# Optimization experiments

Hardware: AMD Instinct MI355X
Metric: run time of the kernel (lower is better)

## Reference

```python
import jax, jax.numpy as jnp
import numpy as np

HID = 1024
NEG = -1e10


def setup_inputs() -> dict:
    key = jax.random.key(0)
    ks = jax.random.split(key, 8)
    batch, src_len = 64, 512
    hidden = jax.random.normal(ks[0], (batch, HID), dtype=jnp.float32)
    encoder_outputs = jax.random.normal(ks[1], (src_len, batch, 2 * HID), dtype=jnp.float32)
    mask = jax.random.randint(ks[2], (batch, src_len), 0, 2).astype(bool)
    # params (torch Linear: y = x @ W.T + b)
    sW = 1.0 / np.sqrt(HID)
    sU = 1.0 / np.sqrt(2 * HID)
    W_w = jax.random.uniform(ks[3], (HID, HID), jnp.float32, -sW, sW)
    W_b = jax.random.uniform(ks[4], (HID,), jnp.float32, -sW, sW)
    U_w = jax.random.uniform(ks[5], (HID, 2 * HID), jnp.float32, -sU, sU)
    U_b = jax.random.uniform(ks[6], (HID,), jnp.float32, -sU, sU)
    v_w = jax.random.uniform(ks[7], (1, HID), jnp.float32, -sW, sW)
    return {"hidden": hidden, "encoder_outputs": encoder_outputs, "mask": mask,
            "W_w": W_w, "W_b": W_b, "U_w": U_w, "U_b": U_b, "v_w": v_w}


def reference(hidden, encoder_outputs, mask, W_w, W_b, U_w, U_b, v_w):
    # hidden: [B, H]; encoder_outputs: [S, B, 2H]; mask: [B, S]
    Wh = hidden @ W_w.T + W_b                       # [B, H], broadcast over S
    enc = jnp.transpose(encoder_outputs, (1, 0, 2))  # [B, S, 2H]
    Ue = jnp.einsum('bse,he->bsh', enc, U_w) + U_b   # [B, S, H]
    energy = jnp.tanh(Wh[:, None, :] + Ue) @ v_w[0]  # [B, S]
    energy = jnp.where(mask, NEG, energy)
    return jax.nn.softmax(energy, axis=1)
```

## Files before the change

### kernel.cpp

```cpp
#include <hip/hip_runtime.h>
#include <math.h>

#define HID   1024
#define HID2  2048
#define BATCH 64
#define SRC   512
#define MROWS (SRC * BATCH)
#define NEGV  (-1e10f)

typedef int  i4v __attribute__((ext_vector_type(4)));
typedef float f4v __attribute__((ext_vector_type(4)));

__global__ void zero_energy(float* __restrict__ e) {
    int i = blockIdx.x * 256 + threadIdx.x;
    if (i < MROWS) e[i] = 0.f;
}

__global__ void split_i8(const float* __restrict__ src,
                         signed char* __restrict__ q1b,
                         signed char* __restrict__ q2b,
                         int n16, float s1, float inv_s1, float s2) {
    int i = blockIdx.x * 256 + threadIdx.x;
    if (i >= n16) return;
    const float4* s = (const float4*)src + (size_t)i * 4;
    float v[16];
    *(float4*)&v[0]  = s[0];
    *(float4*)&v[4]  = s[1];
    *(float4*)&v[8]  = s[2];
    *(float4*)&v[12] = s[3];
    unsigned w1[4], w2[4];
#pragma unroll
    for (int p = 0; p < 4; ++p) {
        unsigned a1 = 0, a2 = 0;
#pragma unroll
        for (int j = 0; j < 4; ++j) {
            float a  = v[p * 4 + j];
            float q1 = rintf(a * s1);
            q1 = fminf(fmaxf(q1, -127.f), 127.f);
            float r  = fmaf(q1, -inv_s1, a);
            float q2 = rintf(r * s2);
            q2 = fminf(fmaxf(q2, -127.f), 127.f);
            a1 |= ((unsigned)((int)q1 & 0xff)) << (8 * j);
            a2 |= ((unsigned)((int)q2 & 0xff)) << (8 * j);
        }
        w1[p] = a1; w2[p] = a2;
    }
    ((uint4*)q1b)[i] = make_uint4(w1[0], w1[1], w1[2], w1[3]);
    ((uint4*)q2b)[i] = make_uint4(w2[0], w2[1], w2[2], w2[3]);
}

__global__ void quant_i8(const float* __restrict__ src,
                         signed char* __restrict__ qb,
                         int n16, float s) {
    int i = blockIdx.x * 256 + threadIdx.x;
    if (i >= n16) return;
    const float4* sp = (const float4*)src + (size_t)i * 4;
    float v[16];
    *(float4*)&v[0]  = sp[0];
    *(float4*)&v[4]  = sp[1];
    *(float4*)&v[8]  = sp[2];
    *(float4*)&v[12] = sp[3];
    unsigned w[4];
#pragma unroll
    for (int p = 0; p < 4; ++p) {
        unsigned a = 0;
#pragma unroll
        for (int j = 0; j < 4; ++j) {
            float q = rintf(v[p * 4 + j] * s);
            q = fminf(fmaxf(q, -127.f), 127.f);
            a |= ((unsigned)((int)q & 0xff)) << (8 * j);
        }
        w[p] = a;
    }
    ((uint4*)qb)[i] = make_uint4(w[0], w[1], w[2], w[3]);
}

__global__ void wh_kernel(const float* __restrict__ hidden,
                          const float* __restrict__ W_w,
                          const float* __restrict__ W_b,
                          float* __restrict__ Wh) {
    __shared__ float sh[HID];
    const int b = blockIdx.y;
    const int t = threadIdx.x;
    for (int k = t; k < HID; k += 256) sh[k] = hidden[b * HID + k];
    __syncthreads();
    const int h = blockIdx.x * 256 + t;
    const float* wr = W_w + (size_t)h * HID;
    float acc = 0.f;
    for (int k = 0; k < HID; k += 4) {
        float4 w = *(const float4*)(wr + k);
        acc += sh[k] * w.x + sh[k+1] * w.y + sh[k+2] * w.z + sh[k+3] * w.w;
    }
    Wh[b * HID + h] = acc + W_b[h];
}

static __device__ __forceinline__ float tanh_fast(float x) {
    float ax = fabsf(x);
    float t  = __expf(-2.f * ax);
    float r  = __fdividef(1.f - t, 1.f + t);
    return copysignf(r, x);
}

__global__ __launch_bounds__(256, 2)
void gemm_energy(const signed char* __restrict__ A1,
                 const signed char* __restrict__ A2,
                 const signed char* __restrict__ B1,
                 const float* __restrict__ Ub,
                 const float* __restrict__ vw,
                 const float* __restrict__ Wh,
                 float* __restrict__ energy,
                 int m_base)
{
    __shared__ signed char sA1[128 * 64];
    __shared__ signed char sA2[128 * 64];
    __shared__ signed char sB1[128 * 64];

    const int tid  = threadIdx.x;
    const int wave = tid >> 6;
    const int lane = tid & 63;

    const int nwg = (int)(gridDim.x * gridDim.y);
    const int bid = (int)(blockIdx.y * gridDim.x + blockIdx.x);
    const int cpx = nwg >> 3;
    const int swz = (bid & 7) * cpx + (bid >> 3);
    const int h0 = (swz & 7) * 128;
    const int m0 = (swz >> 3) * 128;

    const int wm = wave & 1;
    const int wn = wave >> 1;

    i4v c1[4][4], c2[4][4];
#pragma unroll
    for (int i = 0; i < 4; i++)
#pragma unroll
        for (int j = 0; j < 4; j++) {
            c1[i][j] = (i4v){0, 0, 0, 0};
            c2[i][j] = (i4v){0, 0, 0, 0};
        }

    const int ar   = lane & 15;
    const int koff = (lane >> 4) * 16;

    for (int k0 = 0; k0 < HID2; k0 += 64) {
#pragma unroll
        for (int it = 0; it < 2; ++it) {
            const int f    = it * 256 + tid;
            const int row  = f >> 2;
            const int inn  = (f & 3) * 16;
            const int loff = (it * 256 + wave * 64) * 16;

            const signed char* ga = A1 + (size_t)(m0 + row) * HID2 + k0 + inn;
            __builtin_amdgcn_global_load_lds(
                (const __attribute__((address_space(1))) unsigned int*)ga,
                (__attribute__((address_space(3))) unsigned int*)(sA1 + loff),
                16, 0, 0);
            const signed char* gb = A2 + (size_t)(m0 + row) * HID2 + k0 + inn;
            __builtin_amdgcn_global_load_lds(
                (const __attribute__((address_space(1))) unsigned int*)gb,
                (__attribute__((address_space(3))) unsigned int*)(sA2 + loff),
                16, 0, 0);
            const signed char* gc = B1 + (size_t)(h0 + row) * HID2 + k0 + inn;
            __builtin_amdgcn_global_load_lds(
                (const __attribute__((address_space(1))) unsigned int*)gc,
                (__attribute__((address_space(3))) unsigned int*)(sB1 + loff),
                16, 0, 0);
        }
        __syncthreads();

        i4v a1[4], a2[4], b1[4];
#pragma unroll
        for (int i = 0; i < 4; ++i) {
            a1[i] = *(const i4v*)&sA1[(wm * 64 + i * 16 + ar) * 64 + koff];
            a2[i] = *(const i4v*)&sA2[(wm * 64 + i * 16 + ar) * 64 + koff];
            b1[i] = *(const i4v*)&sB1[(wn * 64 + i * 16 + ar) * 64 + koff];
        }
#pragma unroll
        for (int i = 0; i < 4; ++i)
#pragma unroll
            for (int j = 0; j < 4; ++j) {
                c1[i][j] = __builtin_amdgcn_mfma_i32_16x16x64_i8(a1[i], b1[j], c1[i][j], 0, 0, 0);
                c2[i][j] = __builtin_amdgcn_mfma_i32_16x16x64_i8(a2[i], b1[j], c2[i][j], 0, 0, 0);
            }
        __syncthreads();
    }

    const int col = lane & 15;
    const int rg  = lane >> 4;
    const float invs = 1.f / (4096.f * 5746.f);
    float vj[4], ubj[4];
#pragma unroll
    for (int j = 0; j < 4; ++j) {
        const int hc = h0 + wn * 64 + j * 16 + col;
        vj[j]  = vw[hc];
        ubj[j] = Ub[hc];
    }
#pragma unroll
    for (int i = 0; i < 4; ++i) {
#pragma unroll
        for (int r = 0; r < 4; ++r) {
            const int mm = m0 + wm * 64 + i * 16 + rg * 4 + r;
            const int b  = (m_base + mm) & 63;
            const float* whr = Wh + b * HID + h0 + wn * 64 + col;
            float e = 0.f;
#pragma unroll
            for (int j = 0; j < 4; ++j) {
                float C = fmaf((float)c1[i][j][r], 256.f, (float)c2[i][j][r]) * invs;
                float x = C + ubj[j] + whr[j * 16];
                e += vj[j] * tanh_fast(x);
            }
            e += __shfl_xor(e, 1, 64);
            e += __shfl_xor(e, 2, 64);
            e += __shfl_xor(e, 4, 64);
            e += __shfl_xor(e, 8, 64);
            if (col == 0) atomicAdd(&energy[m_base + mm], e);
        }
    }
}

__global__ void softmax_kernel(const float* __restrict__ energy,
                               const int* __restrict__ mask,
                               float* __restrict__ out) {
    const int b = blockIdx.x;
    const int t = threadIdx.x;
    __shared__ float wmax[4], wsum[4];

    float x0 = energy[t * 64 + b];
    float x1 = energy[(t + 256) * 64 + b];
    float e0 = mask[b * SRC + t]       ? NEGV : x0;
    float e1 = mask[b * SRC + t + 256] ? NEGV : x1;

    float mx = fmaxf(e0, e1);
#pragma unroll
    for (int off = 1; off < 64; off <<= 1)
        mx = fmaxf(mx, __shfl_xor(mx, off, 64));
    const int wid = t >> 6, lane = t & 63;
    if (lane == 0) wmax[wid] = mx;
    __syncthreads();
    mx = fmaxf(fmaxf(wmax[0], wmax[1]), fmaxf(wmax[2], wmax[3]));

    float p0 = expf(e0 - mx), p1 = expf(e1 - mx);
    float sum = p0 + p1;
#pragma unroll
    for (int off = 1; off < 64; off <<= 1)
        sum += __shfl_xor(sum, off, 64);
    if (lane == 0) wsum[wid] = sum;
    __syncthreads();
    sum = wsum[0] + wsum[1] + wsum[2] + wsum[3];
    const float inv = 1.f / sum;
    out[b * SRC + t]       = p0 * inv;
    out[b * SRC + t + 256] = p1 * inv;
}

extern "C" void kernel_launch(void* const* d_in, const int* in_sizes, int n_in,
                              void* d_out, int out_size, void* d_ws, size_t ws_size,
                              hipStream_t stream) {
    const float* hidden = (const float*)d_in[0];
    const float* enc    = (const float*)d_in[1];
    const int*   mask   = (const int*)d_in[2];
    const float* W_w    = (const float*)d_in[3];
    const float* W_b    = (const float*)d_in[4];
    const float* U_w    = (const float*)d_in[5];
    const float* U_b    = (const float*)d_in[6];
    const float* v_w    = (const float*)d_in[7];
    float* out = (float*)d_out;

    char* p = (char*)d_ws;
    float* Wh     = (float*)p;             p += (size_t)BATCH * HID * 4;
    float* energy = (float*)p;             p += (size_t)MROWS * 4;
    signed char* B1 = (signed char*)p;     p += (size_t)HID * HID2;
    const size_t fixed = (size_t)(p - (char*)d_ws);

    int R = 1024;
    const int cand[6] = {32768, 16384, 8192, 4096, 2048, 1024};
    for (int c = 0; c < 6; ++c) {
        if (fixed + (size_t)cand[c] * HID2 * 2 <= ws_size) { R = cand[c]; break; }
    }
    signed char* A1 = (signed char*)p;
    signed char* A2 = A1 + (size_t)R * HID2;

    const float Sa1 = 16.f, iSa1 = 1.f / 16.f, Sa2 = 4096.f;
    const float Sb1 = 5746.f;

    hipLaunchKernelGGL(zero_energy, dim3(MROWS / 256), dim3(256), 0, stream, energy);
    hipLaunchKernelGGL(wh_kernel, dim3(4, BATCH), dim3(256), 0, stream,
                       hidden, W_w, W_b, Wh);
    {
        const int n16 = HID * HID2 / 16;
        hipLaunchKernelGGL(quant_i8, dim3((n16 + 255) / 256), dim3(256), 0, stream,
                           U_w, B1, n16, Sb1);
    }
    for (int c0 = 0; c0 < MROWS; c0 += R) {
        const int n16 = R * HID2 / 16;
        hipLaunchKernelGGL(split_i8, dim3((n16 + 255) / 256), dim3(256), 0, stream,
                           enc + (size_t)c0 * HID2, A1, A2, n16, Sa1, iSa1, Sa2);
        hipLaunchKernelGGL(gemm_energy, dim3(HID / 128, R / 128), dim3(256), 0, stream,
                           A1, A2, B1, U_b, v_w, Wh, energy, c0);
    }
    hipLaunchKernelGGL(softmax_kernel, dim3(BATCH), dim3(256), 0, stream,
                       energy, mask, out);
}
```

Baseline: 626.4 us.

## Double-buffer int8 GEMM LDS tiles with XOR swizzle and prefetch

Replaces the single-buffered LDS staging in the int8 MFMA energy GEMM with two buffers, so the next K-slice is loaded with global_load_lds while the current one feeds the MFMAs. It also XOR-swizzles the 16-byte chunk offsets to reduce LDS bank conflicts, raises launch_bounds occupancy from 2 to 3, and sets wave priority around the MFMA block. LDS use doubles to 48KB per block, which may limit how many blocks actually fit, and the tighter register budget could cause spills.

```diff
diff --git a/kernel.cpp b/kernel.cpp
--- a/kernel.cpp
+++ b/kernel.cpp
@@ -101,7 +101,7 @@
     return copysignf(r, x);
 }
 
-__global__ __launch_bounds__(256, 2)
+__global__ __launch_bounds__(256, 3)
 void gemm_energy(const signed char* __restrict__ A1,
                  const signed char* __restrict__ A2,
                  const signed char* __restrict__ B1,
@@ -111,9 +111,7 @@
                  float* __restrict__ energy,
                  int m_base)
 {
-    __shared__ signed char sA1[128 * 64];
-    __shared__ signed char sA2[128 * 64];
-    __shared__ signed char sB1[128 * 64];
+    __shared__ signed char sAll[2 * 3 * 8192];
 
     const int tid  = threadIdx.x;
     const int wave = tid >> 6;
@@ -138,42 +136,57 @@
             c2[i][j] = (i4v){0, 0, 0, 0};
         }
 
-    const int ar   = lane & 15;
-    const int koff = (lane >> 4) * 16;
-
-    for (int k0 = 0; k0 < HID2; k0 += 64) {
-#pragma unroll
-        for (int it = 0; it < 2; ++it) {
-            const int f    = it * 256 + tid;
-            const int row  = f >> 2;
-            const int inn  = (f & 3) * 16;
-            const int loff = (it * 256 + wave * 64) * 16;
-
-            const signed char* ga = A1 + (size_t)(m0 + row) * HID2 + k0 + inn;
-            __builtin_amdgcn_global_load_lds(
-                (const __attribute__((address_space(1))) unsigned int*)ga,
-                (__attribute__((address_space(3))) unsigned int*)(sA1 + loff),
-                16, 0, 0);
-            const signed char* gb = A2 + (size_t)(m0 + row) * HID2 + k0 + inn;
-            __builtin_amdgcn_global_load_lds(
-                (const __attribute__((address_space(1))) unsigned int*)gb,
-                (__attribute__((address_space(3))) unsigned int*)(sA2 + loff),
-                16, 0, 0);
-            const signed char* gc = B1 + (size_t)(h0 + row) * HID2 + k0 + inn;
-            __builtin_amdgcn_global_load_lds(
-                (const __attribute__((address_space(1))) unsigned int*)gc,
-                (__attribute__((address_space(3))) unsigned int*)(sB1 + loff),
-                16, 0, 0);
-        }
-        __syncthreads();
+    const int ar = lane & 15;
+    const int ko = (((lane >> 4) ^ ((ar >> 1) & 3)) * 16);
+
+#define STAGE_TILES(CB, K0)                                                   \
+    {                                                                         \
+        _Pragma("unroll")                                                     \
+        for (int it = 0; it < 2; ++it) {                                      \
+            const int f    = it * 256 + tid;                                  \
+            const int row  = f >> 2;                                          \
+            const int inn  = (((f & 3) ^ ((row >> 1) & 3))) * 16;             \
+            const int loff = (CB) + (it * 256 + wave * 64) * 16;              \
+            const signed char* ga = A1 + (size_t)(m0 + row) * HID2 + (K0) + inn; \
+            __builtin_amdgcn_global_load_lds(                                 \
+                (const __attribute__((address_space(1))) unsigned int*)ga,    \
+                (__attribute__((address_space(3))) unsigned int*)(sAll + loff), \
+                16, 0, 0);                                                    \
+            const signed char* gb = A2 + (size_t)(m0 + row) * HID2 + (K0) + inn; \
+            __builtin_amdgcn_global_load_lds(                                 \
+                (const __attribute__((address_space(1))) unsigned int*)gb,    \
+                (__attribute__((address_space(3))) unsigned int*)(sAll + 8192 + loff), \
+                16, 0, 0);                                                    \
+            const signed char* gc = B1 + (size_t)(h0 + row) * HID2 + (K0) + inn; \
+            __builtin_amdgcn_global_load_lds(                                 \
+                (const __attribute__((address_space(1))) unsigned int*)gc,    \
+                (__attribute__((address_space(3))) unsigned int*)(sAll + 16384 + loff), \
+                16, 0, 0);                                                    \
+        }                                                                     \
+    }
+
+    STAGE_TILES(0, 0);
+    asm volatile("s_waitcnt vmcnt(0)" ::: "memory");
+    __builtin_amdgcn_s_barrier();
+
+    int cur = 0;
+    for (int ks = 0; ks < 32; ++ks) {
+        const int cb = cur * 24576;
+        if (ks + 1 < 32) STAGE_TILES(cb ^ 24576, (ks + 1) * 64);
 
         i4v a1[4], a2[4], b1[4];
 #pragma unroll
         for (int i = 0; i < 4; ++i) {
-            a1[i] = *(const i4v*)&sA1[(wm * 64 + i * 16 + ar) * 64 + koff];
-            a2[i] = *(const i4v*)&sA2[(wm * 64 + i * 16 + ar) * 64 + koff];
-            b1[i] = *(const i4v*)&sB1[(wn * 64 + i * 16 + ar) * 64 + koff];
-        }
+            const int ra = cb + (wm * 64 + i * 16 + ar) * 64 + ko;
+            const int rb = cb + 16384 + (wn * 64 + i * 16 + ar) * 64 + ko;
+            a1[i] = *(const i4v*)&sAll[ra];
+            a2[i] = *(const i4v*)&sAll[8192 + ra];
+            b1[i] = *(const i4v*)&sAll[rb];
+        }
+        asm volatile("s_waitcnt lgkmcnt(0)" ::: "memory");
+        __builtin_amdgcn_sched_barrier(0);
+
+        __builtin_amdgcn_s_setprio(1);
 #pragma unroll
         for (int i = 0; i < 4; ++i)
 #pragma unroll
@@ -181,8 +194,13 @@
                 c1[i][j] = __builtin_amdgcn_mfma_i32_16x16x64_i8(a1[i], b1[j], c1[i][j], 0, 0, 0);
                 c2[i][j] = __builtin_amdgcn_mfma_i32_16x16x64_i8(a2[i], b1[j], c2[i][j], 0, 0, 0);
             }
-        __syncthreads();
-    }
+        __builtin_amdgcn_s_setprio(0);
+
+        asm volatile("s_waitcnt vmcnt(0)" ::: "memory");
+        __builtin_amdgcn_s_barrier();
+        cur ^= 1;
+    }
+#undef STAGE_TILES
 
     const int col = lane & 15;
     const int rg  = lane >> 4;
```

New measurement: 993.6 us. 1.59x slower.
